# Kernel tuning notes

Measured on AMD Instinct MI355X. Metric: run time of the kernel, lower is better.

## Reference

```python
import jax, jax.numpy as jnp
import numpy as np

B, N, C = 4, 2048, 1024
H = 16
D = C // H  # head_dim = 64
NEG = -1e9


def setup_inputs() -> dict:
    key = jax.random.key(0)
    k1, k2, k3, k4 = jax.random.split(key, 4)
    x = jax.random.normal(k1, (B, N, C), dtype=jnp.float32)
    # additive causal mask [N, N]: 0 on/below diagonal, -1e9 above
    causal = jnp.tril(jnp.ones((N, N), dtype=bool))
    attn_mask = jnp.where(causal, 0.0, NEG).astype(jnp.float32)
    # params: qkv Dense (no bias, qkv_bias=False), proj Dense (with bias)
    W_qkv = jax.random.normal(k2, (C, 3 * C), dtype=jnp.float32) / np.sqrt(C)
    W_proj = jax.random.normal(k3, (C, C), dtype=jnp.float32) / np.sqrt(C)
    b_proj = jnp.zeros((C,), dtype=jnp.float32)
    return {"x": x, "attn_mask": attn_mask, "W_qkv": W_qkv,
            "W_proj": W_proj, "b_proj": b_proj}


def reference(x, attn_mask, W_qkv, W_proj, b_proj):
    b, n, c = x.shape
    # qkv projection -> [B, N, 3, H, D] -> q,k,v each [B, H, N, D]
    qkv = (x @ W_qkv).reshape(b, n, 3, H, D)
    qkv = jnp.transpose(qkv, (2, 0, 3, 1, 4))
    q, k, v = qkv[0], qkv[1], qkv[2]
    # unfused attention: full [B, H, N, N] score matrix
    scores = jnp.einsum('bhnd,bhmd->bhnm', q, k) / np.sqrt(D).astype(jnp.float32)
    scores = scores + attn_mask  # broadcast [N, N] over batch/heads
    attn_w = jax.nn.softmax(scores.astype(jnp.float32), axis=-1).astype(scores.dtype)
    out = jnp.einsum('bhnm,bhmd->bhnd', attn_w, v)
    out = jnp.transpose(out, (0, 2, 1, 3)).reshape(b, n, c)
    return out @ W_proj + b_proj
```

## Files before the change

kernel.cpp:

```cpp
#include <hip/hip_runtime.h>
#include <stdint.h>


typedef short s16x8 __attribute__((ext_vector_type(8)));
typedef float f32x4 __attribute__((ext_vector_type(4)));

__device__ __forceinline__ uint16_t f2bf(float f) {
  union { float f; uint32_t u; } v; v.f = f;
  uint32_t r = v.u + 0x7fffu + ((v.u >> 16) & 1u);
  return (uint16_t)(r >> 16);
}

#define GLOAD_LDS16(g, l)                                            \
  __builtin_amdgcn_global_load_lds(                                  \
      (const __attribute__((address_space(1))) void*)(g),            \
      (__attribute__((address_space(3))) void*)(l), 16, 0, 0)

__global__ __launch_bounds__(256) void cvt_kernel(
    const float* __restrict__ src, uint16_t* __restrict__ dst) {
  const int i = blockIdx.x * 256 + threadIdx.x;
  const f32x4 a = ((const f32x4*)src)[2 * i];
  const f32x4 b = ((const f32x4*)src)[2 * i + 1];
  s16x8 r;
  r[0] = (short)f2bf(a[0]); r[1] = (short)f2bf(a[1]);
  r[2] = (short)f2bf(a[2]); r[3] = (short)f2bf(a[3]);
  r[4] = (short)f2bf(b[0]); r[5] = (short)f2bf(b[1]);
  r[6] = (short)f2bf(b[2]); r[7] = (short)f2bf(b[3]);
  ((s16x8*)dst)[i] = r;
}

__global__ __launch_bounds__(256) void transpose_kernel(
    const float* __restrict__ src, uint16_t* __restrict__ dst, int R, int C) {
  __shared__ uint16_t tile[32][33];
  const int bx = blockIdx.x * 32, by = blockIdx.y * 32;
  const int tx = threadIdx.x & 31, ty = threadIdx.x >> 5;
#pragma unroll
  for (int i = 0; i < 32; i += 8)
    tile[ty + i][tx] = f2bf(src[(size_t)(by + ty + i) * C + bx + tx]);
  __syncthreads();
#pragma unroll
  for (int i = 0; i < 32; i += 8)
    dst[(size_t)(bx + ty + i) * R + by + tx] = tile[tx][ty + i];
}

__global__ __launch_bounds__(256) void vtrans_kernel(
    const uint16_t* __restrict__ src, uint16_t* __restrict__ dst) {
  const int bh = blockIdx.y >> 1, dhalf = blockIdx.y & 1;
  const int n0 = blockIdx.x * 32, d0 = dhalf * 32;
  const uint16_t* sb = src + (size_t)bh * 131072;
  uint16_t* db = dst + (size_t)bh * 131072;
  __shared__ uint16_t tile[32][33];
  const int tx = threadIdx.x & 31, ty = threadIdx.x >> 5;
#pragma unroll
  for (int i = 0; i < 32; i += 8)
    tile[ty + i][tx] = sb[(size_t)(n0 + ty + i) * 64 + d0 + tx];
  __syncthreads();
#pragma unroll
  for (int i = 0; i < 32; i += 8)
    db[(size_t)(d0 + ty + i) * 2048 + n0 + tx] = tile[tx][ty + i];
}

template <bool ROUTE>
__global__ __launch_bounds__(256) void gemm_bt_kernel(
    const uint16_t* __restrict__ A, const uint16_t* __restrict__ Bt,
    float* __restrict__ Cout,
    uint16_t* __restrict__ rq, uint16_t* __restrict__ rk, uint16_t* __restrict__ rv,
    const float* __restrict__ bias, int M, int N, int K) {
  __shared__ uint16_t sA[128 * 32];
  __shared__ uint16_t sB[128 * 32];
  const int tid = threadIdx.x;
  const int lane = tid & 63, w = tid >> 6;
  const int l15 = lane & 15, quad = lane >> 4;
  const int row0 = blockIdx.y * 128, col0 = blockIdx.x * 128;
  const int wm = (w >> 1) * 64, wn = (w & 1) * 64;

  f32x4 acc[4][4];
#pragma unroll
  for (int i = 0; i < 4; ++i)
#pragma unroll
    for (int j = 0; j < 4; ++j)
#pragma unroll
      for (int e = 0; e < 4; ++e) acc[i][j][e] = 0.0f;

  for (int k0 = 0; k0 < K; k0 += 32) {
    __syncthreads();
#pragma unroll
    for (int i = 0; i < 2; ++i) {
      const int cbase = i * 256 + w * 64;
      const int c = cbase + lane;
      const int r = c >> 2, kc = (c & 3) * 8;
      GLOAD_LDS16(A + (size_t)(row0 + r) * K + k0 + kc, sA + cbase * 8);
      GLOAD_LDS16(Bt + (size_t)(col0 + r) * K + k0 + kc, sB + cbase * 8);
    }
    __syncthreads();

    s16x8 aF[4], bF[4];
#pragma unroll
    for (int mt = 0; mt < 4; ++mt)
      aF[mt] = *(const s16x8*)(sA + (wm + mt * 16 + l15) * 32 + quad * 8);
#pragma unroll
    for (int nt = 0; nt < 4; ++nt)
      bF[nt] = *(const s16x8*)(sB + (wn + nt * 16 + l15) * 32 + quad * 8);
#pragma unroll
    for (int mt = 0; mt < 4; ++mt)
#pragma unroll
      for (int nt = 0; nt < 4; ++nt)
        acc[mt][nt] = __builtin_amdgcn_mfma_f32_16x16x32_bf16(aF[mt], bF[nt], acc[mt][nt], 0, 0, 0);
  }

  if (ROUTE) {
    const int which = col0 >> 10;
    uint16_t* dst = (which == 0) ? rq : ((which == 1) ? rk : rv);
#pragma unroll
    for (int mt = 0; mt < 4; ++mt) {
#pragma unroll
      for (int nt = 0; nt < 4; ++nt) {
        const int colg0 = col0 + wn + nt * 16;
        const int h = (colg0 >> 6) & 15, d0 = colg0 & 63;
#pragma unroll
        for (int i = 0; i < 4; ++i) {
          const int rowg = row0 + wm + mt * 16 + quad * 4 + i;
          const int bh = ((rowg >> 11) << 4) + h, n = rowg & 2047;
          dst[(size_t)bh * 131072 + (size_t)n * 64 + d0 + l15] = f2bf(acc[mt][nt][i]);
        }
      }
    }
  } else {
#pragma unroll
    for (int mt = 0; mt < 4; ++mt) {
#pragma unroll
      for (int nt = 0; nt < 4; ++nt) {
        const int colg = col0 + wn + nt * 16 + l15;
        const float bv = bias[colg];
#pragma unroll
        for (int i = 0; i < 4; ++i) {
          const int rowg = row0 + wm + mt * 16 + quad * 4 + i;
          Cout[(size_t)rowg * N + colg] = acc[mt][nt][i] + bv;
        }
      }
    }
  }
}

__global__ __launch_bounds__(256) void attn_kernel(
    const uint16_t* __restrict__ q_ws, const uint16_t* __restrict__ k_ws,
    const uint16_t* __restrict__ vt_ws, uint16_t* __restrict__ out) {
  const int p = blockIdx.x;
  const int bh = blockIdx.y;
  const int b = bh >> 4, h = bh & 15;
  const int q0L = p * 64, q0H = (31 - p) * 64;
  const int tid = threadIdx.x;
  const int lane = tid & 63, w = tid >> 6;
  const int l15 = lane & 15, quad = lane >> 4;

  const uint16_t* qb = q_ws + (size_t)bh * 131072;
  const uint16_t* kb = k_ws + (size_t)bh * 131072;
  const uint16_t* vtb = vt_ws + (size_t)bh * 131072;

  __shared__ uint16_t sK[64 * 72];
  __shared__ uint16_t sV[64 * 72];
  __shared__ uint16_t sP[8][16 * 72];

  const int qrowL = q0L + w * 16 + l15;
  const int qrowH = q0H + w * 16 + l15;
  const s16x8 aQL0 = *(const s16x8*)(qb + (size_t)qrowL * 64 + quad * 8);
  const s16x8 aQL1 = *(const s16x8*)(qb + (size_t)qrowL * 64 + 32 + quad * 8);
  const s16x8 aQH0 = *(const s16x8*)(qb + (size_t)qrowH * 64 + quad * 8);
  const s16x8 aQH1 = *(const s16x8*)(qb + (size_t)qrowH * 64 + 32 + quad * 8);

  float lL[4], lH[4];
  f32x4 oL[4], oH[4];
#pragma unroll
  for (int i = 0; i < 4; ++i) {
    lL[i] = 0.0f; lH[i] = 0.0f;
#pragma unroll
    for (int e = 0; e < 4; ++e) { oL[i][e] = 0.0f; oH[i][e] = 0.0f; }
  }

  const int vr = tid >> 2, dc = (tid & 3) * 16;
  s16x8 rk0 = *(const s16x8*)(kb + (size_t)vr * 64 + dc);
  s16x8 rk1 = *(const s16x8*)(kb + (size_t)vr * 64 + dc + 8);
  s16x8 rv0 = *(const s16x8*)(vtb + (size_t)vr * 2048 + dc);
  s16x8 rv1 = *(const s16x8*)(vtb + (size_t)vr * 2048 + dc + 8);

  const float k2 = 0.18033688011112042f;
  uint16_t* pwH = sP[w];
  uint16_t* pwL = sP[w + 4];

  auto tile = [&](const s16x8& a0, const s16x8& a1, uint16_t* pw, bool diag,
                  f32x4* o, float* lp) {
    f32x4 s[4];
#pragma unroll
    for (int nt = 0; nt < 4; ++nt) {
#pragma unroll
      for (int e = 0; e < 4; ++e) s[nt][e] = 0.0f;
      const s16x8 bK0 = *(const s16x8*)(sK + (nt * 16 + l15) * 72 + quad * 8);
      const s16x8 bK1 = *(const s16x8*)(sK + (nt * 16 + l15) * 72 + 32 + quad * 8);
      s[nt] = __builtin_amdgcn_mfma_f32_16x16x32_bf16(a0, bK0, s[nt], 0, 0, 0);
      s[nt] = __builtin_amdgcn_mfma_f32_16x16x32_bf16(a1, bK1, s[nt], 0, 0, 0);
    }
#pragma unroll
    for (int nt = 0; nt < 4; ++nt) {
      const int coll = nt * 16 + l15;
#pragma unroll
      for (int i = 0; i < 4; ++i) {
        const bool masked = diag && (coll > (w * 16 + quad * 4 + i));
        const float pp = masked ? 0.0f : exp2f(fmaf(s[nt][i], k2, -12.0f));
        lp[i] += pp;
        pw[(quad * 4 + i) * 72 + coll] = f2bf(pp);
      }
    }
#pragma unroll
    for (int dblk = 0; dblk < 4; ++dblk) {
#pragma unroll
      for (int kk = 0; kk < 2; ++kk) {
        const s16x8 aP = *(const s16x8*)(pw + l15 * 72 + kk * 32 + quad * 8);
        const s16x8 bV = *(const s16x8*)(sV + (dblk * 16 + l15) * 72 + kk * 32 + quad * 8);
        o[dblk] = __builtin_amdgcn_mfma_f32_16x16x32_bf16(aP, bV, o[dblk], 0, 0, 0);
      }
    }
  };

  for (int kv0 = 0; kv0 <= q0H; kv0 += 64) {
    __syncthreads();
    *(s16x8*)(sK + vr * 72 + dc) = rk0;
    *(s16x8*)(sK + vr * 72 + dc + 8) = rk1;
    *(s16x8*)(sV + vr * 72 + dc) = rv0;
    *(s16x8*)(sV + vr * 72 + dc + 8) = rv1;
    __syncthreads();

    if (kv0 + 64 <= q0H) {
      const int kvn = kv0 + 64;
      rk0 = *(const s16x8*)(kb + (size_t)(kvn + vr) * 64 + dc);
      rk1 = *(const s16x8*)(kb + (size_t)(kvn + vr) * 64 + dc + 8);
      rv0 = *(const s16x8*)(vtb + (size_t)vr * 2048 + kvn + dc);
      rv1 = *(const s16x8*)(vtb + (size_t)vr * 2048 + kvn + dc + 8);
    }

    tile(aQH0, aQH1, pwH, kv0 == q0H, oH, lH);
    if (kv0 <= q0L) tile(aQL0, aQL1, pwL, kv0 == q0L, oL, lL);
  }

  const size_t obase = (size_t)b * 2048 * 1024 + (size_t)h * 64;
  auto epi = [&](f32x4* o, float* lp, int q0) {
#pragma unroll
    for (int i = 0; i < 4; ++i) {
      float l = lp[i];
#pragma unroll
      for (int off = 8; off >= 1; off >>= 1) l += __shfl_xor(l, off, 16);
      const float inv = 1.0f / l;
      const int row = q0 + w * 16 + quad * 4 + i;
#pragma unroll
      for (int dblk = 0; dblk < 4; ++dblk)
        out[obase + (size_t)row * 1024 + dblk * 16 + l15] = f2bf(o[dblk][i] * inv);
    }
  };
  epi(oH, lH, q0H);
  epi(oL, lL, q0L);
}

extern "C" void kernel_launch(void* const* d_in, const int* in_sizes, int n_in,
                              void* d_out, int out_size, void* d_ws, size_t ws_size,
                              hipStream_t stream) {
  (void)in_sizes; (void)n_in; (void)out_size; (void)ws_size;
  const float* x     = (const float*)d_in[0];
  const float* Wqkv  = (const float*)d_in[2];
  const float* Wproj = (const float*)d_in[3];
  const float* bproj = (const float*)d_in[4];
  float* outp = (float*)d_out;

  uint16_t* ws      = (uint16_t*)d_ws;
  uint16_t* q_ws    = ws;
  uint16_t* k_ws    = ws + (size_t)8388608;
  uint16_t* v_ws    = ws + (size_t)16777216;
  uint16_t* attn_ws = ws + (size_t)16777216;
  uint16_t* vt_ws   = ws + (size_t)25165824;
  uint16_t* wqkvT   = ws + (size_t)25165824;
  uint16_t* wprojT  = ws + (size_t)8388608;
  uint16_t* xbf     = (uint16_t*)d_out;

  cvt_kernel<<<4096, 256, 0, stream>>>(x, xbf);
  transpose_kernel<<<dim3(96, 32), 256, 0, stream>>>(Wqkv, wqkvT, 1024, 3072);
  gemm_bt_kernel<true><<<dim3(24, 64), 256, 0, stream>>>(
      xbf, wqkvT, nullptr, q_ws, k_ws, v_ws, nullptr, 8192, 3072, 1024);
  vtrans_kernel<<<dim3(64, 128), 256, 0, stream>>>(v_ws, vt_ws);
  attn_kernel<<<dim3(16, 64), 256, 0, stream>>>(q_ws, k_ws, vt_ws, attn_ws);
  transpose_kernel<<<dim3(32, 32), 256, 0, stream>>>(Wproj, wprojT, 1024, 1024);
  gemm_bt_kernel<false><<<dim3(8, 64), 256, 0, stream>>>(
      attn_ws, wprojT, outp, nullptr, nullptr, nullptr, bproj, 8192, 1024, 1024);
}
```

Baseline: 311.3 us.

## Transpose QK^T MFMA operands so each lane owns one query row

The QK^T MFMA now takes K as the A operand and Q as the B operand, so each lane holds the scores for one query row across four consecutive keys. The row sum becomes a single scalar per lane and the bf16 P values are packed two at a time and written with 8-byte LDS stores instead of scalar 16-bit stores. The K fragments are loaded once and shared by the high and low query tiles, and the V fragments are shared in the PV loop. This is meant to cut LDS traffic, the shuffle reductions and the conversion instructions. It also switches to a cheaper rounding in the bf16 pack and holds more values in registers at once.

```diff
diff --git a/kernel.cpp b/kernel.cpp
--- a/kernel.cpp
+++ b/kernel.cpp
@@ -4,11 +4,22 @@
 
 typedef short s16x8 __attribute__((ext_vector_type(8)));
 typedef float f32x4 __attribute__((ext_vector_type(4)));
+typedef uint32_t u32x2 __attribute__((ext_vector_type(2)));
 
 __device__ __forceinline__ uint16_t f2bf(float f) {
   union { float f; uint32_t u; } v; v.f = f;
   uint32_t r = v.u + 0x7fffu + ((v.u >> 16) & 1u);
   return (uint16_t)(r >> 16);
+}
+
+__device__ __forceinline__ uint32_t pkbf(float a, float b) {
+  union { float f; uint32_t u; } x, y; x.f = a; y.f = b;
+  const uint32_t xu = x.u + 0x8000u, yu = y.u + 0x8000u;
+#if __has_builtin(__builtin_amdgcn_perm)
+  return __builtin_amdgcn_perm(yu, xu, 0x07060302u);
+#else
+  return (xu >> 16) | (yu & 0xffff0000u);
+#endif
 }
 
 #define GLOAD_LDS16(g, l)                                            \
@@ -168,14 +179,12 @@
   const s16x8 aQH0 = *(const s16x8*)(qb + (size_t)qrowH * 64 + quad * 8);
   const s16x8 aQH1 = *(const s16x8*)(qb + (size_t)qrowH * 64 + 32 + quad * 8);
 
-  float lL[4], lH[4];
-  f32x4 oL[4], oH[4];
-#pragma unroll
-  for (int i = 0; i < 4; ++i) {
-    lL[i] = 0.0f; lH[i] = 0.0f;
-#pragma unroll
-    for (int e = 0; e < 4; ++e) { oL[i][e] = 0.0f; oH[i][e] = 0.0f; }
-  }
+  float lH = 0.0f, lL = 0.0f;
+  f32x4 oH[4], oL[4];
+#pragma unroll
+  for (int i = 0; i < 4; ++i)
+#pragma unroll
+    for (int e = 0; e < 4; ++e) { oH[i][e] = 0.0f; oL[i][e] = 0.0f; }
 
   const int vr = tid >> 2, dc = (tid & 3) * 16;
   s16x8 rk0 = *(const s16x8*)(kb + (size_t)vr * 64 + dc);
@@ -186,40 +195,10 @@
   const float k2 = 0.18033688011112042f;
   uint16_t* pwH = sP[w];
   uint16_t* pwL = sP[w + 4];
-
-  auto tile = [&](const s16x8& a0, const s16x8& a1, uint16_t* pw, bool diag,
-                  f32x4* o, float* lp) {
-    f32x4 s[4];
-#pragma unroll
-    for (int nt = 0; nt < 4; ++nt) {
-#pragma unroll
-      for (int e = 0; e < 4; ++e) s[nt][e] = 0.0f;
-      const s16x8 bK0 = *(const s16x8*)(sK + (nt * 16 + l15) * 72 + quad * 8);
-      const s16x8 bK1 = *(const s16x8*)(sK + (nt * 16 + l15) * 72 + 32 + quad * 8);
-      s[nt] = __builtin_amdgcn_mfma_f32_16x16x32_bf16(a0, bK0, s[nt], 0, 0, 0);
-      s[nt] = __builtin_amdgcn_mfma_f32_16x16x32_bf16(a1, bK1, s[nt], 0, 0, 0);
-    }
-#pragma unroll
-    for (int nt = 0; nt < 4; ++nt) {
-      const int coll = nt * 16 + l15;
-#pragma unroll
-      for (int i = 0; i < 4; ++i) {
-        const bool masked = diag && (coll > (w * 16 + quad * 4 + i));
-        const float pp = masked ? 0.0f : exp2f(fmaf(s[nt][i], k2, -12.0f));
-        lp[i] += pp;
-        pw[(quad * 4 + i) * 72 + coll] = f2bf(pp);
-      }
-    }
-#pragma unroll
-    for (int dblk = 0; dblk < 4; ++dblk) {
-#pragma unroll
-      for (int kk = 0; kk < 2; ++kk) {
-        const s16x8 aP = *(const s16x8*)(pw + l15 * 72 + kk * 32 + quad * 8);
-        const s16x8 bV = *(const s16x8*)(sV + (dblk * 16 + l15) * 72 + kk * 32 + quad * 8);
-        o[dblk] = __builtin_amdgcn_mfma_f32_16x16x32_bf16(aP, bV, o[dblk], 0, 0, 0);
-      }
-    }
-  };
+  const int pwr = l15 * 72 + quad * 4;
+  const int prd = l15 * 72 + quad * 8;
+
+  const int qlocal = w * 16 + l15;
 
   for (int kv0 = 0; kv0 <= q0H; kv0 += 64) {
     __syncthreads();
@@ -237,22 +216,86 @@
       rv1 = *(const s16x8*)(vtb + (size_t)vr * 2048 + kvn + dc + 8);
     }
 
-    tile(aQH0, aQH1, pwH, kv0 == q0H, oH, lH);
-    if (kv0 <= q0L) tile(aQL0, aQL1, pwL, kv0 == q0L, oL, lL);
+    const bool doL = (kv0 <= q0L);
+    const bool dgH = (kv0 == q0H), dgL = (kv0 == q0L);
+
+    s16x8 bK0[4], bK1[4];
+#pragma unroll
+    for (int nt = 0; nt < 4; ++nt) {
+      bK0[nt] = *(const s16x8*)(sK + (nt * 16 + l15) * 72 + quad * 8);
+      bK1[nt] = *(const s16x8*)(sK + (nt * 16 + l15) * 72 + 32 + quad * 8);
+    }
+
+    f32x4 sH[4], sL[4];
+#pragma unroll
+    for (int nt = 0; nt < 4; ++nt) {
+#pragma unroll
+      for (int e = 0; e < 4; ++e) { sH[nt][e] = 0.0f; sL[nt][e] = 0.0f; }
+      sH[nt] = __builtin_amdgcn_mfma_f32_16x16x32_bf16(bK0[nt], aQH0, sH[nt], 0, 0, 0);
+      sH[nt] = __builtin_amdgcn_mfma_f32_16x16x32_bf16(bK1[nt], aQH1, sH[nt], 0, 0, 0);
+      if (doL) {
+        sL[nt] = __builtin_amdgcn_mfma_f32_16x16x32_bf16(bK0[nt], aQL0, sL[nt], 0, 0, 0);
+        sL[nt] = __builtin_amdgcn_mfma_f32_16x16x32_bf16(bK1[nt], aQL1, sL[nt], 0, 0, 0);
+      }
+    }
+
+#pragma unroll
+    for (int nt = 0; nt < 4; ++nt) {
+      const int kvb = nt * 16 + quad * 4;
+      float pv[4];
+#pragma unroll
+      for (int i = 0; i < 4; ++i) {
+        const bool masked = dgH && (kvb + i > qlocal);
+        pv[i] = masked ? 0.0f : exp2f(fmaf(sH[nt][i], k2, -12.0f));
+        lH += pv[i];
+      }
+      *(u32x2*)(pwH + pwr + nt * 16) = u32x2{pkbf(pv[0], pv[1]), pkbf(pv[2], pv[3])};
+    }
+    if (doL) {
+#pragma unroll
+      for (int nt = 0; nt < 4; ++nt) {
+        const int kvb = nt * 16 + quad * 4;
+        float pv[4];
+#pragma unroll
+        for (int i = 0; i < 4; ++i) {
+          const bool masked = dgL && (kvb + i > qlocal);
+          pv[i] = masked ? 0.0f : exp2f(fmaf(sL[nt][i], k2, -12.0f));
+          lL += pv[i];
+        }
+        *(u32x2*)(pwL + pwr + nt * 16) = u32x2{pkbf(pv[0], pv[1]), pkbf(pv[2], pv[3])};
+      }
+    }
+
+    const s16x8 pH0 = *(const s16x8*)(pwH + prd);
+    const s16x8 pH1 = *(const s16x8*)(pwH + prd + 32);
+    const s16x8 pL0 = doL ? *(const s16x8*)(pwL + prd) : s16x8{0};
+    const s16x8 pL1 = doL ? *(const s16x8*)(pwL + prd + 32) : s16x8{0};
+#pragma unroll
+    for (int dblk = 0; dblk < 4; ++dblk) {
+      const s16x8 v0 = *(const s16x8*)(sV + (dblk * 16 + l15) * 72 + quad * 8);
+      const s16x8 v1 = *(const s16x8*)(sV + (dblk * 16 + l15) * 72 + 32 + quad * 8);
+      oH[dblk] = __builtin_amdgcn_mfma_f32_16x16x32_bf16(pH0, v0, oH[dblk], 0, 0, 0);
+      oH[dblk] = __builtin_amdgcn_mfma_f32_16x16x32_bf16(pH1, v1, oH[dblk], 0, 0, 0);
+      if (doL) {
+        oL[dblk] = __builtin_amdgcn_mfma_f32_16x16x32_bf16(pL0, v0, oL[dblk], 0, 0, 0);
+        oL[dblk] = __builtin_amdgcn_mfma_f32_16x16x32_bf16(pL1, v1, oL[dblk], 0, 0, 0);
+      }
+    }
   }
 
   const size_t obase = (size_t)b * 2048 * 1024 + (size_t)h * 64;
-  auto epi = [&](f32x4* o, float* lp, int q0) {
+  auto epi = [&](f32x4* o, float lacc, int q0) {
+    float l = lacc;
+    l += __shfl_xor(l, 16);
+    l += __shfl_xor(l, 32);
+    const float inv = 1.0f / l;
 #pragma unroll
     for (int i = 0; i < 4; ++i) {
-      float l = lp[i];
-#pragma unroll
-      for (int off = 8; off >= 1; off >>= 1) l += __shfl_xor(l, off, 16);
-      const float inv = 1.0f / l;
+      const float inv_i = __shfl(inv, quad * 4 + i, 16);
       const int row = q0 + w * 16 + quad * 4 + i;
 #pragma unroll
       for (int dblk = 0; dblk < 4; ++dblk)
-        out[obase + (size_t)row * 1024 + dblk * 16 + l15] = f2bf(o[dblk][i] * inv);
+        out[obase + (size_t)row * 1024 + dblk * 16 + l15] = f2bf(o[dblk][i] * inv_i);
     }
   };
   epi(oH, lH, q0H);
```

Result: slower. 319.9 us (+2.7%).
